# Kernel tuning notes

Measured on AMD Instinct MI355X. Metric: run time of the kernel, lower is better.

The kernel has to match this reference:

```python
import jax, jax.numpy as jnp
import numpy as np

B = 1024        # number of graphs in the batch
D = 256         # per-type node feature dim
DG = 128        # global (direct-cat) feature dim
N_ATOM = 65536
N_BOND = 131072
N_ITERS = 6


def _lstm_step(q_star, h, c, W_ih, W_hh, b_ih, b_hh):
    # torch LSTM gate order: i, f, g, o
    gates = q_star @ W_ih.T + b_ih + h @ W_hh.T + b_hh  # [B, 4D]
    i, f, g, o = jnp.split(gates, 4, axis=-1)
    c = jax.nn.sigmoid(f) * c + jax.nn.sigmoid(i) * jnp.tanh(g)
    h = jax.nn.sigmoid(o) * jnp.tanh(c)
    return h, c


def _set2set(feat, seg, W_ih, W_hh, b_ih, b_hh, n_iters, batch_size):
    d = feat.shape[1]
    h = jnp.zeros((batch_size, d), feat.dtype)
    c = jnp.zeros((batch_size, d), feat.dtype)
    q_star = jnp.zeros((batch_size, 2 * d), feat.dtype)
    for _ in range(n_iters):
        h, c = _lstm_step(q_star, h, c, W_ih, W_hh, b_ih, b_hh)
        q = h  # [B, D]
        # per-node attention logit: e_i = x_i . q_{seg(i)}
        e = jnp.sum(feat * q[seg], axis=-1)  # [N]
        # segment softmax (stable)
        m = jax.ops.segment_max(e, seg, num_segments=batch_size)
        ex = jnp.exp(e - m[seg])
        denom = jax.ops.segment_sum(ex, seg, num_segments=batch_size)
        alpha = ex / denom[seg]  # [N]
        # weighted readout per graph
        r = jax.ops.segment_sum(feat * alpha[:, None], seg, num_segments=batch_size)  # [B, D]
        q_star = jnp.concatenate([q, r], axis=-1)
    return q_star  # [B, 2D]


def setup_inputs() -> dict:
    key = jax.random.key(0)
    ks = jax.random.split(key, 12)
    s = 1.0 / np.sqrt(D)  # torch LSTM init range
    inp = {
        "feat_atom": jax.random.normal(ks[0], (N_ATOM, D), jnp.float32),
        "seg_atom": (jnp.arange(N_ATOM) // (N_ATOM // B)).astype(jnp.int32),
        "feat_bond": jax.random.normal(ks[1], (N_BOND, D), jnp.float32),
        "seg_bond": (jnp.arange(N_BOND) // (N_BOND // B)).astype(jnp.int32),
        "feat_global": jax.random.normal(ks[2], (B, DG), jnp.float32),
        "W_ih_atom": jax.random.uniform(ks[3], (4 * D, 2 * D), jnp.float32, -s, s),
        "W_hh_atom": jax.random.uniform(ks[4], (4 * D, D), jnp.float32, -s, s),
        "b_ih_atom": jax.random.uniform(ks[5], (4 * D,), jnp.float32, -s, s),
        "b_hh_atom": jax.random.uniform(ks[6], (4 * D,), jnp.float32, -s, s),
        "W_ih_bond": jax.random.uniform(ks[7], (4 * D, 2 * D), jnp.float32, -s, s),
        "W_hh_bond": jax.random.uniform(ks[8], (4 * D, D), jnp.float32, -s, s),
        "b_ih_bond": jax.random.uniform(ks[9], (4 * D,), jnp.float32, -s, s),
        "b_hh_bond": jax.random.uniform(ks[10], (4 * D,), jnp.float32, -s, s),
    }
    return inp


def reference(feat_atom, seg_atom, feat_bond, seg_bond, feat_global,
              W_ih_atom, W_hh_atom, b_ih_atom, b_hh_atom,
              W_ih_bond, W_hh_bond, b_ih_bond, b_hh_bond):
    qa = _set2set(feat_atom, seg_atom, W_ih_atom, W_hh_atom, b_ih_atom, b_hh_atom, N_ITERS, B)
    qb = _set2set(feat_bond, seg_bond, W_ih_bond, W_hh_bond, b_ih_bond, b_hh_bond, N_ITERS, B)
    return jnp.concatenate([qa, qb, feat_global], axis=-1)  # [B, 2D + 2D + DG]
```

## Files before the change

kernel.cpp:

```cpp
#include <hip/hip_runtime.h>
#include <stdint.h>

#define NGRAPH 1024
#define DFEAT  256
#define KATOM  64
#define KBOND  128

typedef __attribute__((ext_vector_type(4))) float accv_t;
typedef __attribute__((ext_vector_type(8))) short bfrag_t;
typedef __attribute__((ext_vector_type(4))) unsigned short upk4_t;
typedef __attribute__((ext_vector_type(8))) unsigned short upk8_t;
typedef __attribute__((ext_vector_type(4))) unsigned int u32x4;

__device__ __forceinline__ unsigned short f2bf(float f) {
    union { float f; unsigned int u; } v; v.f = f;
    return (unsigned short)((v.u + 0x7FFFu + ((v.u >> 16) & 1u)) >> 16);
}
__device__ __forceinline__ float bf2f(unsigned short h) {
    union { unsigned int u; float f; } v; v.u = ((unsigned int)h) << 16;
    return v.f;
}
__device__ __forceinline__ float sigm(float x) { return 1.0f / (1.0f + __expf(-x)); }
__device__ __forceinline__ float tanh_f(float x) {
    float e = __expf(2.0f * x);
    return 1.0f - 2.0f / (e + 1.0f);
}
__device__ __forceinline__ unsigned int packq(float a, float b, float c, float d, float inv) {
    int q0 = (int)rintf(a * inv), q1 = (int)rintf(b * inv);
    int q2 = (int)rintf(c * inv), q3 = (int)rintf(d * inv);
    return (unsigned int)(q0 & 0xFF) | ((unsigned int)(q1 & 0xFF) << 8)
         | ((unsigned int)(q2 & 0xFF) << 16) | ((unsigned int)(q3 & 0xFF) << 24);
}
__device__ __forceinline__ void dec16(const unsigned int* h, float* x) {
    #pragma unroll
    for (int w4 = 0; w4 < 4; ++w4) {
        unsigned int u = h[w4];
        x[w4 * 4 + 0] = (float)((int)(u << 24) >> 24);
        x[w4 * 4 + 1] = (float)((int)(u << 16) >> 24);
        x[w4 * 4 + 2] = (float)((int)(u << 8)  >> 24);
        x[w4 * 4 + 3] = (float)((int)u >> 24);
    }
}

__global__ __launch_bounds__(256) void k_cvtprep(
    const float* __restrict__ fA, const float* __restrict__ fB,
    unsigned int* __restrict__ oA, unsigned int* __restrict__ oB,
    float* __restrict__ scA, float* __restrict__ scB,
    const float* __restrict__ WihA, const float* __restrict__ WhhA,
    const float* __restrict__ bihA, const float* __restrict__ bhhA,
    const float* __restrict__ WihB, const float* __restrict__ WhhB,
    const float* __restrict__ bihB, const float* __restrict__ bhhB,
    unsigned short* __restrict__ Wc, float* __restrict__ bsum, int doquant)
{
    int bid = blockIdx.x;
    if (bid < 1024) {
        if (!doquant) return;
        int wid  = bid * 4 + (threadIdx.x >> 6);
        int lane = threadIdx.x & 63;
        int grp  = lane >> 3;
        #pragma unroll 2
        for (int n = wid; n < 65536; n += 4096) {
            accv_t v = __builtin_nontemporal_load((const accv_t*)(fA + (size_t)n * 256) + lane);
            float m = fmaxf(fmaxf(fabsf(v[0]), fabsf(v[1])), fmaxf(fabsf(v[2]), fabsf(v[3])));
            m = fmaxf(m, __shfl_xor(m, 1));
            m = fmaxf(m, __shfl_xor(m, 2));
            m = fmaxf(m, __shfl_xor(m, 4));
            float inv = (m > 0.0f) ? 127.0f / m : 0.0f;
            oA[(size_t)n * 64 + lane] = packq(v[0], v[1], v[2], v[3], inv);
            if ((lane & 7) == 0) scA[(size_t)n * 8 + grp] = m * (1.0f / 127.0f);
        }
        #pragma unroll 2
        for (int n = wid; n < 131072; n += 4096) {
            accv_t v = __builtin_nontemporal_load((const accv_t*)(fB + (size_t)n * 256) + lane);
            float m = fmaxf(fmaxf(fabsf(v[0]), fabsf(v[1])), fmaxf(fabsf(v[2]), fabsf(v[3])));
            m = fmaxf(m, __shfl_xor(m, 1));
            m = fmaxf(m, __shfl_xor(m, 2));
            m = fmaxf(m, __shfl_xor(m, 4));
            float inv = (m > 0.0f) ? 127.0f / m : 0.0f;
            oB[(size_t)n * 64 + lane] = packq(v[0], v[1], v[2], v[3], inv);
            if ((lane & 7) == 0) scB[(size_t)n * 8 + grp] = m * (1.0f / 127.0f);
        }
    } else {
        int pid = bid - 1024;
        int set = pid >> 10;
        int n   = pid & 1023;
        int k   = threadIdx.x;
        const float* Wih = set ? WihB : WihA;
        const float* Whh = set ? WhhB : WhhA;
        float w1 = Wih[(size_t)n * 512 + k] + Whh[(size_t)n * 256 + k];
        float w2 = Wih[(size_t)n * 512 + 256 + k];
        size_t base = ((size_t)(set << 10) + n) * 512;
        Wc[base + k]       = f2bf(w1);
        Wc[base + 256 + k] = f2bf(w2);
        if (k == 0) {
            const float* bih = set ? bihB : bihA;
            const float* bhh = set ? bhhB : bhhA;
            bsum[(set << 10) + n] = bih[n] + bhh[n];
        }
    }
}

__global__ __launch_bounds__(256) void k_gemm(
    const unsigned short* __restrict__ hrb, const unsigned short* __restrict__ Wc,
    const float* __restrict__ bsum, unsigned short* __restrict__ gates)
{
    __shared__ unsigned short sA[64 * 40];
    __shared__ unsigned short sB[64 * 40];

    int set   = blockIdx.x >> 8;
    int qq    = blockIdx.x & 255;
    int mbase = (qq >> 4) * 64;
    int nbase = (qq & 15) * 64;
    int t     = threadIdx.x;
    int lane  = t & 63;
    int w     = t >> 6;
    int wrow  = (w >> 1) * 32;
    int wcol  = (w & 1) * 32;
    int l15   = lane & 15;
    int khalf = (lane >> 4) * 8;

    const unsigned short* Am = hrb + (size_t)(set << 10) * 512;
    const unsigned short* Bm = Wc  + (size_t)(set << 10) * 512;

    accv_t acc[2][2];
    #pragma unroll
    for (int i = 0; i < 2; ++i)
        #pragma unroll
        for (int j = 0; j < 2; ++j)
            acc[i][j] = (accv_t){0.f, 0.f, 0.f, 0.f};

    int srow = t >> 2;
    int skc  = (t & 3) * 8;
    for (int k0 = 0; k0 < 512; k0 += 32) {
        *(upk8_t*)&sA[srow * 40 + skc] =
            *(const upk8_t*)&Am[(size_t)(mbase + srow) * 512 + k0 + skc];
        *(upk8_t*)&sB[srow * 40 + skc] =
            *(const upk8_t*)&Bm[(size_t)(nbase + srow) * 512 + k0 + skc];
        __syncthreads();

        bfrag_t a_f[2], b_f[2];
        #pragma unroll
        for (int i = 0; i < 2; ++i)
            a_f[i] = *(const bfrag_t*)&sA[(wrow + i * 16 + l15) * 40 + khalf];
        #pragma unroll
        for (int j = 0; j < 2; ++j)
            b_f[j] = *(const bfrag_t*)&sB[(wcol + j * 16 + l15) * 40 + khalf];
        #pragma unroll
        for (int i = 0; i < 2; ++i)
            #pragma unroll
            for (int j = 0; j < 2; ++j)
                acc[i][j] = __builtin_amdgcn_mfma_f32_16x16x32_bf16(a_f[i], b_f[j], acc[i][j], 0, 0, 0);
        __syncthreads();
    }

    int r4 = (lane >> 4) * 4;
    #pragma unroll
    for (int i = 0; i < 2; ++i) {
        #pragma unroll
        for (int j = 0; j < 2; ++j) {
            int col  = nbase + wcol + j * 16 + l15;
            float bs = bsum[(set << 10) + col];
            #pragma unroll
            for (int v = 0; v < 2; ++v) {
                int row0 = mbase + wrow + i * 16 + r4 + 2 * v;
                gates[((size_t)(set << 10) + row0) * 1024 + col]     = f2bf(acc[i][j][2 * v] + bs);
                gates[((size_t)(set << 10) + row0 + 1) * 1024 + col] = f2bf(acc[i][j][2 * v + 1] + bs);
            }
        }
    }
}

template <int MODE, bool LAST>
__global__ __launch_bounds__(256) void k_attn(
    const float* __restrict__ featA, const float* __restrict__ featB,
    const unsigned int* __restrict__ i8A, const unsigned int* __restrict__ i8B,
    const float* __restrict__ scA, const float* __restrict__ scB,
    const unsigned short* __restrict__ gates, const float* __restrict__ bsum,
    unsigned short* __restrict__ hrb, float* __restrict__ cst,
    const float* __restrict__ fgp, float* __restrict__ outp, int iter)
{
    __shared__ float qv[256];
    __shared__ float sw_s[16], cw_s[16];
    __shared__ float racc_s[16][260];

    int bid = blockIdx.x;
    int set = (bid < 1024) ? 1 : 0;
    int b   = bid & 1023;
    int K   = set ? KBOND : KATOM;
    int t = threadIdx.x;
    size_t sb = (size_t)(set << 10) + b;
    size_t ob = (size_t)b * 1152 + (set ? 512 : 0);

    {
        int d = t;
        float gi, gf, gg, go, cold;
        if (iter == 0) {
            gi = bsum[(set << 10) + d];
            gf = bsum[(set << 10) + 256 + d];
            gg = bsum[(set << 10) + 512 + d];
            go = bsum[(set << 10) + 768 + d];
            cold = 0.0f;
        } else {
            const unsigned short* gp = gates + sb * 1024;
            gi = bf2f(gp[d]); gf = bf2f(gp[256 + d]);
            gg = bf2f(gp[512 + d]); go = bf2f(gp[768 + d]);
            cold = cst[sb * 256 + d];
        }
        float cn = sigm(gf) * cold + sigm(gi) * tanh_f(gg);
        float h  = sigm(go) * tanh_f(cn);
        if (LAST) { outp[ob + d] = h; }
        else      { cst[sb * 256 + d] = cn; hrb[sb * 512 + d] = f2bf(h); }
        qv[d] = h;
    }
    __syncthreads();

    int lane = t & 63;
    int wv   = t >> 6;
    int g    = lane >> 4;
    int s    = lane & 15;
    int npw  = K >> 2;
    int nq   = npw >> 2;
    int node0 = wv * npw + g;
    float C = 0.0f, sacc = 0.0f;
    int pid = (wv << 2) | g;

    if (MODE == 1) {
        const unsigned int* fb = (set ? i8B : i8A)
                               + ((size_t)b * K + node0) * 64 + s * 4;
        const float* scp = (set ? scB : scA)
                         + ((size_t)b * K + node0) * 8 + (s >> 1);

        float qr[16];
        #pragma unroll
        for (int j = 0; j < 16; ++j) qr[j] = qv[s * 16 + j];
        float r[16];
        #pragma unroll
        for (int j = 0; j < 16; ++j) r[j] = 0.0f;

        #pragma unroll 4
        for (int qd = 0; qd < nq; ++qd) {
            u32x4 hx = *(const u32x4*)(fb + (size_t)qd * 256);
            float sc = scp[(size_t)qd * 32];
            float x[16];
            dec16((const unsigned int*)&hx, x);
            float e = 0.0f;
            #pragma unroll
            for (int j = 0; j < 16; ++j) e += x[j] * qr[j];
            e *= sc;
            e += __shfl_xor(e, 1);
            e += __shfl_xor(e, 2);
            e += __shfl_xor(e, 4);
            e += __shfl_xor(e, 8);
            float w = (qd == 0) ? 1.0f : __expf(e - C);
            if (qd == 0) C = e;
            sacc += w;
            float wl = w * sc;
            #pragma unroll
            for (int j = 0; j < 16; ++j) r[j] += wl * x[j];
        }
        #pragma unroll
        for (int j = 0; j < 16; j += 4)
            *(float4*)&racc_s[pid][s * 16 + j] = *(float4*)&r[j];
    } else {
        const float* feat = set ? featB : featA;
        const float* fb = feat + ((size_t)b * K + node0) * 256 + s * 4;
        float4 q0 = *(const float4*)&qv[s*4];
        float4 q1 = *(const float4*)&qv[64  + s*4];
        float4 q2 = *(const float4*)&qv[128 + s*4];
        float4 q3 = *(const float4*)&qv[192 + s*4];
        float4 r0 = make_float4(0.f,0.f,0.f,0.f), r1 = r0, r2 = r0, r3 = r0;
        #pragma unroll 2
        for (int qd = 0; qd < nq; ++qd) {
            const float* p = fb + (size_t)qd * 1024;
            float4 x0 = *(const float4*)(p);
            float4 x1 = *(const float4*)(p + 64);
            float4 x2 = *(const float4*)(p + 128);
            float4 x3 = *(const float4*)(p + 192);
            float e = x0.x*q0.x + x0.y*q0.y + x0.z*q0.z + x0.w*q0.w
                    + x1.x*q1.x + x1.y*q1.y + x1.z*q1.z + x1.w*q1.w
                    + x2.x*q2.x + x2.y*q2.y + x2.z*q2.z + x2.w*q2.w
                    + x3.x*q3.x + x3.y*q3.y + x3.z*q3.z + x3.w*q3.w;
            e += __shfl_xor(e, 1); e += __shfl_xor(e, 2);
            e += __shfl_xor(e, 4); e += __shfl_xor(e, 8);
            float w = (qd == 0) ? 1.0f : __expf(e - C);
            if (qd == 0) C = e;
            sacc += w;
            r0.x += w*x0.x; r0.y += w*x0.y; r0.z += w*x0.z; r0.w += w*x0.w;
            r1.x += w*x1.x; r1.y += w*x1.y; r1.z += w*x1.z; r1.w += w*x1.w;
            r2.x += w*x2.x; r2.y += w*x2.y; r2.z += w*x2.z; r2.w += w*x2.w;
            r3.x += w*x3.x; r3.y += w*x3.y; r3.z += w*x3.z; r3.w += w*x3.w;
        }
        *(float4*)&racc_s[pid][s*4]       = r0;
        *(float4*)&racc_s[pid][64  + s*4] = r1;
        *(float4*)&racc_s[pid][128 + s*4] = r2;
        *(float4*)&racc_s[pid][192 + s*4] = r3;
    }
    if (s == 0) { sw_s[pid] = sacc; cw_s[pid] = C; }
    __syncthreads();

    {
        float Cm = cw_s[0];
        #pragma unroll
        for (int p2 = 1; p2 < 16; ++p2) Cm = fmaxf(Cm, cw_s[p2]);
        float S = 0.0f, r = 0.0f;
        #pragma unroll
        for (int p2 = 0; p2 < 16; ++p2) {
            float f = __expf(cw_s[p2] - Cm);
            S += sw_s[p2] * f;
            r += racc_s[p2][t] * f;
        }
        float rv = r / S;
        if (LAST) {
            outp[ob + 256 + t] = rv;
            if (set && t < 128)
                outp[(size_t)b * 1152 + 1024 + t] = fgp[(size_t)b * 128 + t];
        } else {
            hrb[sb * 512 + 256 + t] = f2bf(rv);
        }
    }
}

extern "C" void kernel_launch(void* const* d_in, const int* in_sizes, int n_in,
                              void* d_out, int out_size, void* d_ws, size_t ws_size,
                              hipStream_t stream) {
    const float* feat_atom   = (const float*)d_in[0];
    const float* feat_bond   = (const float*)d_in[2];
    const float* feat_global = (const float*)d_in[4];
    const float* WihA = (const float*)d_in[5];
    const float* WhhA = (const float*)d_in[6];
    const float* bihA = (const float*)d_in[7];
    const float* bhhA = (const float*)d_in[8];
    const float* WihB = (const float*)d_in[9];
    const float* WhhB = (const float*)d_in[10];
    const float* bihB = (const float*)d_in[11];
    const float* bhhB = (const float*)d_in[12];
    float* out = (float*)d_out;

    char* ws = (char*)d_ws;
    unsigned short* Wc    = (unsigned short*)(ws + 0);
    float*          bsum  = (float*)(ws + 2097152);
    unsigned short* gates = (unsigned short*)(ws + 2105344);
    unsigned short* hrb   = (unsigned short*)(ws + 6299648);
    float*          cst   = (float*)(ws + 8396800);
    unsigned int*   i8A   = (unsigned int*)(ws + 10493952);
    unsigned int*   i8B   = (unsigned int*)(ws + 27271168);
    float*          scA   = (float*)(ws + 60825600);
    float*          scB   = (float*)(ws + 62922752);
    const size_t WS_NEED = 62922752 + 4194304;
    (void)in_sizes; (void)n_in; (void)out_size;

    bool i8 = (ws_size >= WS_NEED);

    k_cvtprep<<<3072, 256, 0, stream>>>(feat_atom, feat_bond, i8A, i8B, scA, scB,
                                        WihA, WhhA, bihA, bhhA,
                                        WihB, WhhB, bihB, bhhB,
                                        Wc, bsum, i8 ? 1 : 0);
    if (i8) {
        k_attn<1, false><<<2048, 256, 0, stream>>>(feat_atom, feat_bond, i8A, i8B,
                                                   scA, scB, gates, bsum, hrb, cst,
                                                   feat_global, out, 0);
        for (int it = 1; it < 5; ++it) {
            k_gemm<<<512, 256, 0, stream>>>(hrb, Wc, bsum, gates);
            k_attn<1, false><<<2048, 256, 0, stream>>>(feat_atom, feat_bond, i8A, i8B,
                                                       scA, scB, gates, bsum, hrb, cst,
                                                       feat_global, out, it);
        }
        k_gemm<<<512, 256, 0, stream>>>(hrb, Wc, bsum, gates);
        k_attn<1, true><<<2048, 256, 0, stream>>>(feat_atom, feat_bond, i8A, i8B,
                                                  scA, scB, gates, bsum, hrb, cst,
                                                  feat_global, out, 5);
    } else {
        k_attn<2, false><<<2048, 256, 0, stream>>>(feat_atom, feat_bond, 0, 0, 0, 0,
                                                   gates, bsum, hrb, cst,
                                                   feat_global, out, 0);
        for (int it = 1; it < 5; ++it) {
            k_gemm<<<512, 256, 0, stream>>>(hrb, Wc, bsum, gates);
            k_attn<2, false><<<2048, 256, 0, stream>>>(feat_atom, feat_bond, 0, 0, 0, 0,
                                                       gates, bsum, hrb, cst,
                                                       feat_global, out, it);
        }
        k_gemm<<<512, 256, 0, stream>>>(hrb, Wc, bsum, gates);
        k_attn<2, true><<<2048, 256, 0, stream>>>(feat_atom, feat_bond, 0, 0, 0, 0,
                                                  gates, bsum, hrb, cst,
                                                  feat_global, out, 5);
    }
}
```

Baseline: 185.6 us.

## Fuse LSTM cell update into gate GEMM epilogue via permuted weight rows

Weight rows are permuted so each 64-column GEMM tile holds the i,f,g,o gates for the same 16 hidden units, which lets the GEMM epilogue compute the LSTM cell and hidden state directly. This removes the bf16 gates buffer round trip through global memory and the gate math in the attention kernel. h is double-buffered across iterations because the GEMM reads the previous h while writing the new one. Risk: the wave layout changes to 16x64 per wave, with more B-fragment LDS reads per wave.

```diff
diff --git a/kernel.cpp b/kernel.cpp
--- a/kernel.cpp
+++ b/kernel.cpp
@@ -84,12 +84,15 @@
         int pid = bid - 1024;
         int set = pid >> 10;
         int n   = pid & 1023;
+        int g0  = n >> 8;
+        int d0  = n & 255;
+        int nr  = ((d0 >> 4) << 6) + (g0 << 4) + (d0 & 15);
         int k   = threadIdx.x;
         const float* Wih = set ? WihB : WihA;
         const float* Whh = set ? WhhB : WhhA;
         float w1 = Wih[(size_t)n * 512 + k] + Whh[(size_t)n * 256 + k];
         float w2 = Wih[(size_t)n * 512 + 256 + k];
-        size_t base = ((size_t)(set << 10) + n) * 512;
+        size_t base = ((size_t)(set << 10) + nr) * 512;
         Wc[base + k]       = f2bf(w1);
         Wc[base + 256 + k] = f2bf(w2);
         if (k == 0) {
@@ -100,9 +103,11 @@
     }
 }
 
+template <bool LAST>
 __global__ __launch_bounds__(256) void k_gemm(
-    const unsigned short* __restrict__ hrb, const unsigned short* __restrict__ Wc,
-    const float* __restrict__ bsum, unsigned short* __restrict__ gates)
+    const unsigned short* __restrict__ hprev, const unsigned short* __restrict__ Wc,
+    const float* __restrict__ bsum, float* __restrict__ cst,
+    unsigned short* __restrict__ hcur, float* __restrict__ outp)
 {
     __shared__ unsigned short sA[64 * 40];
     __shared__ unsigned short sB[64 * 40];
@@ -114,20 +119,16 @@
     int t     = threadIdx.x;
     int lane  = t & 63;
     int w     = t >> 6;
-    int wrow  = (w >> 1) * 32;
-    int wcol  = (w & 1) * 32;
+    int wrow  = w << 4;
     int l15   = lane & 15;
     int khalf = (lane >> 4) * 8;
 
-    const unsigned short* Am = hrb + (size_t)(set << 10) * 512;
-    const unsigned short* Bm = Wc  + (size_t)(set << 10) * 512;
-
-    accv_t acc[2][2];
+    const unsigned short* Am = hprev + (size_t)(set << 10) * 512;
+    const unsigned short* Bm = Wc    + (size_t)(set << 10) * 512;
+
+    accv_t acc[4];
     #pragma unroll
-    for (int i = 0; i < 2; ++i)
-        #pragma unroll
-        for (int j = 0; j < 2; ++j)
-            acc[i][j] = (accv_t){0.f, 0.f, 0.f, 0.f};
+    for (int j = 0; j < 4; ++j) acc[j] = (accv_t){0.f, 0.f, 0.f, 0.f};
 
     int srow = t >> 2;
     int skc  = (t & 3) * 8;
@@ -138,35 +139,38 @@
             *(const upk8_t*)&Bm[(size_t)(nbase + srow) * 512 + k0 + skc];
         __syncthreads();
 
-        bfrag_t a_f[2], b_f[2];
-        #pragma unroll
-        for (int i = 0; i < 2; ++i)
-            a_f[i] = *(const bfrag_t*)&sA[(wrow + i * 16 + l15) * 40 + khalf];
-        #pragma unroll
-        for (int j = 0; j < 2; ++j)
-            b_f[j] = *(const bfrag_t*)&sB[(wcol + j * 16 + l15) * 40 + khalf];
-        #pragma unroll
-        for (int i = 0; i < 2; ++i)
-            #pragma unroll
-            for (int j = 0; j < 2; ++j)
-                acc[i][j] = __builtin_amdgcn_mfma_f32_16x16x32_bf16(a_f[i], b_f[j], acc[i][j], 0, 0, 0);
+        bfrag_t a_f = *(const bfrag_t*)&sA[(wrow + l15) * 40 + khalf];
+        bfrag_t b_f[4];
+        #pragma unroll
+        for (int j = 0; j < 4; ++j)
+            b_f[j] = *(const bfrag_t*)&sB[(j * 16 + l15) * 40 + khalf];
+        #pragma unroll
+        for (int j = 0; j < 4; ++j)
+            acc[j] = __builtin_amdgcn_mfma_f32_16x16x32_bf16(a_f, b_f[j], acc[j], 0, 0, 0);
         __syncthreads();
     }
 
-    int r4 = (lane >> 4) * 4;
+    int r4   = (lane >> 4) * 4;
+    int d    = (nbase >> 2) + l15;
+    int sb10 = set << 10;
+    float bi = bsum[sb10 + d];
+    float bf_ = bsum[sb10 + 256 + d];
+    float bg = bsum[sb10 + 512 + d];
+    float bo = bsum[sb10 + 768 + d];
     #pragma unroll
-    for (int i = 0; i < 2; ++i) {
-        #pragma unroll
-        for (int j = 0; j < 2; ++j) {
-            int col  = nbase + wcol + j * 16 + l15;
-            float bs = bsum[(set << 10) + col];
-            #pragma unroll
-            for (int v = 0; v < 2; ++v) {
-                int row0 = mbase + wrow + i * 16 + r4 + 2 * v;
-                gates[((size_t)(set << 10) + row0) * 1024 + col]     = f2bf(acc[i][j][2 * v] + bs);
-                gates[((size_t)(set << 10) + row0 + 1) * 1024 + col] = f2bf(acc[i][j][2 * v + 1] + bs);
-            }
-        }
+    for (int v = 0; v < 4; ++v) {
+        int graph  = mbase + wrow + r4 + v;
+        size_t gi_ = (size_t)sb10 + graph;
+        float cold = cst[gi_ * 256 + d];
+        float xi = acc[0][v] + bi;
+        float xf = acc[1][v] + bf_;
+        float xg = acc[2][v] + bg;
+        float xo = acc[3][v] + bo;
+        float cn = sigm(xf) * cold + sigm(xi) * tanh_f(xg);
+        float h  = sigm(xo) * tanh_f(cn);
+        if (!LAST) cst[gi_ * 256 + d] = cn;
+        hcur[gi_ * 512 + d] = f2bf(h);
+        if (LAST) outp[(size_t)graph * 1152 + (set ? 512 : 0) + d] = h;
     }
 }
 
@@ -175,9 +179,9 @@
     const float* __restrict__ featA, const float* __restrict__ featB,
     const unsigned int* __restrict__ i8A, const unsigned int* __restrict__ i8B,
     const float* __restrict__ scA, const float* __restrict__ scB,
-    const unsigned short* __restrict__ gates, const float* __restrict__ bsum,
-    unsigned short* __restrict__ hrb, float* __restrict__ cst,
-    const float* __restrict__ fgp, float* __restrict__ outp, int iter)
+    const float* __restrict__ bsum, unsigned short* __restrict__ hrcur,
+    float* __restrict__ cst, const float* __restrict__ fgp,
+    float* __restrict__ outp, int iter)
 {
     __shared__ float qv[256];
     __shared__ float sw_s[16], cw_s[16];
@@ -193,24 +197,19 @@
 
     {
         int d = t;
-        float gi, gf, gg, go, cold;
         if (iter == 0) {
-            gi = bsum[(set << 10) + d];
-            gf = bsum[(set << 10) + 256 + d];
-            gg = bsum[(set << 10) + 512 + d];
-            go = bsum[(set << 10) + 768 + d];
-            cold = 0.0f;
+            float gi = bsum[(set << 10) + d];
+            float gf = bsum[(set << 10) + 256 + d];
+            float gg = bsum[(set << 10) + 512 + d];
+            float go = bsum[(set << 10) + 768 + d];
+            float cn = sigm(gi) * tanh_f(gg);
+            float h  = sigm(go) * tanh_f(cn);
+            cst[sb * 256 + d]   = cn;
+            hrcur[sb * 512 + d] = f2bf(h);
+            qv[d] = h;
         } else {
-            const unsigned short* gp = gates + sb * 1024;
-            gi = bf2f(gp[d]); gf = bf2f(gp[256 + d]);
-            gg = bf2f(gp[512 + d]); go = bf2f(gp[768 + d]);
-            cold = cst[sb * 256 + d];
-        }
-        float cn = sigm(gf) * cold + sigm(gi) * tanh_f(gg);
-        float h  = sigm(go) * tanh_f(cn);
-        if (LAST) { outp[ob + d] = h; }
-        else      { cst[sb * 256 + d] = cn; hrb[sb * 512 + d] = f2bf(h); }
-        qv[d] = h;
+            qv[d] = bf2f(hrcur[sb * 512 + d]);
+        }
     }
     __syncthreads();
 
@@ -315,7 +314,7 @@
             if (set && t < 128)
                 outp[(size_t)b * 1152 + 1024 + t] = fgp[(size_t)b * 128 + t];
         } else {
-            hrb[sb * 512 + 256 + t] = f2bf(rv);
+            hrcur[sb * 512 + 256 + t] = f2bf(rv);
         }
     }
 }
@@ -337,16 +336,16 @@
     float* out = (float*)d_out;
 
     char* ws = (char*)d_ws;
-    unsigned short* Wc    = (unsigned short*)(ws + 0);
-    float*          bsum  = (float*)(ws + 2097152);
-    unsigned short* gates = (unsigned short*)(ws + 2105344);
-    unsigned short* hrb   = (unsigned short*)(ws + 6299648);
-    float*          cst   = (float*)(ws + 8396800);
-    unsigned int*   i8A   = (unsigned int*)(ws + 10493952);
-    unsigned int*   i8B   = (unsigned int*)(ws + 27271168);
-    float*          scA   = (float*)(ws + 60825600);
-    float*          scB   = (float*)(ws + 62922752);
-    const size_t WS_NEED = 62922752 + 4194304;
+    unsigned short* Wc   = (unsigned short*)(ws + 0);
+    float*          bsum = (float*)(ws + 2097152);
+    float*          cst  = (float*)(ws + 2105344);
+    unsigned short* hrb0 = (unsigned short*)(ws + 4202496);
+    unsigned short* hrb1 = (unsigned short*)(ws + 6299648);
+    unsigned int*   i8A  = (unsigned int*)(ws + 8396800);
+    unsigned int*   i8B  = (unsigned int*)(ws + 25174016);
+    float*          scA  = (float*)(ws + 58728448);
+    float*          scB  = (float*)(ws + 60825600);
+    const size_t WS_NEED = 60825600 + 4194304;
     (void)in_sizes; (void)n_in; (void)out_size;
 
     bool i8 = (ws_size >= WS_NEED);
@@ -357,31 +356,35 @@
                                         Wc, bsum, i8 ? 1 : 0);
     if (i8) {
         k_attn<1, false><<<2048, 256, 0, stream>>>(feat_atom, feat_bond, i8A, i8B,
-                                                   scA, scB, gates, bsum, hrb, cst,
+                                                   scA, scB, bsum, hrb0, cst,
                                                    feat_global, out, 0);
         for (int it = 1; it < 5; ++it) {
-            k_gemm<<<512, 256, 0, stream>>>(hrb, Wc, bsum, gates);
+            unsigned short* prev = (it & 1) ? hrb0 : hrb1;
+            unsigned short* cur  = (it & 1) ? hrb1 : hrb0;
+            k_gemm<false><<<512, 256, 0, stream>>>(prev, Wc, bsum, cst, cur, out);
             k_attn<1, false><<<2048, 256, 0, stream>>>(feat_atom, feat_bond, i8A, i8B,
-                                                       scA, scB, gates, bsum, hrb, cst,
+                                                       scA, scB, bsum, cur, cst,
                                                        feat_global, out, it);
         }
-        k_gemm<<<512, 256, 0, stream>>>(hrb, Wc, bsum, gates);
+        k_gemm<true><<<512, 256, 0, stream>>>(hrb0, Wc, bsum, cst, hrb1, out);
         k_attn<1, true><<<2048, 256, 0, stream>>>(feat_atom, feat_bond, i8A, i8B,
-                                                  scA, scB, gates, bsum, hrb, cst,
+                                                  scA, scB, bsum, hrb1, cst,
                                                   feat_global, out, 5);
     } else {
         k_attn<2, false><<<2048, 256, 0, stream>>>(feat_atom, feat_bond, 0, 0, 0, 0,
-                                                   gates, bsum, hrb, cst,
+                                                   bsum, hrb0, cst,
                                                    feat_global, out, 0);
         for (int it = 1; it < 5; ++it) {
-            k_gemm<<<512, 256, 0, stream>>>(hrb, Wc, bsum, gates);
+            unsigned short* prev = (it & 1) ? hrb0 : hrb1;
+            unsigned short* cur  = (it & 1) ? hrb1 : hrb0;
+            k_gemm<false><<<512, 256, 0, stream>>>(prev, Wc, bsum, cst, cur, out);
             k_attn<2, false><<<2048, 256, 0, stream>>>(feat_atom, feat_bond, 0, 0, 0, 0,
-                                                       gates, bsum, hrb, cst,
+                                                       bsum, cur, cst,
                                                        feat_global, out, it);
         }
-        k_gemm<<<512, 256, 0, stream>>>(hrb, Wc, bsum, gates);
+        k_gemm<true><<<512, 256, 0, stream>>>(hrb0, Wc, bsum, cst, hrb1, out);
         k_attn<2, true><<<2048, 256, 0, stream>>>(feat_atom, feat_bond, 0, 0, 0, 0,
-                                                  gates, bsum, hrb, cst,
+                                                  bsum, hrb1, cst,
                                                   feat_global, out, 5);
     }
 }
```

Result: no change. 188.8 us (+1.7%).
